# Optimization experiments

Measured on AMD Instinct MI355X. Metric: run time of the kernel, lower is better.

The kernel has to match this reference:

```python
import jax, jax.numpy as jnp
import numpy as np


def setup_inputs() -> dict:
    key = jax.random.key(0)
    k1, k2, k3, k4, k5 = jax.random.split(key, 5)
    N, K, F, N_up = 300000, 6, 64, 75000
    features = jax.random.normal(k1, (N, F), dtype=jnp.float32)
    weight = jax.random.uniform(k2, (N, 1), dtype=jnp.float32)
    nweights = jax.random.uniform(k3, (N, K), dtype=jnp.float32)
    nidx = jax.random.randint(k4, (N, K), 0, N, dtype=jnp.int32)
    sel_idx_up = jax.random.randint(k5, (N_up, 1), 0, N, dtype=jnp.int32)
    return {"features": features, "weight": weight, "nweights": nweights,
            "nidx": nidx, "sel_idx_up": sel_idx_up}


def reference(features, weight, nweights, nidx, sel_idx_up):
    # PushUp(mode='mean', add_self=False) with weight provided.
    N, F = features.shape
    w = jax.nn.relu(weight)                      # weights forced >= 0
    up_f = features * w                          # [N, F]
    up_f = jnp.concatenate([w, up_f], axis=-1)   # mean mode: prepend weight channel -> [N, F+1]

    # push_sum: each node i pushes nweights[i,k] * up_f[i] to node nidx[i,k]
    valid = (nidx >= 0)                          # -1 entries are masked (none here, kept for fidelity)
    safe_idx = jnp.where(valid, nidx, 0)         # [N, K]
    contrib = (nweights * valid.astype(up_f.dtype))[..., None] * up_f[:, None, :]  # [N, K, F+1]
    pushed = jnp.zeros((N, F + 1), dtype=up_f.dtype).at[safe_idx.reshape(-1)].add(
        contrib.reshape(-1, F + 1))              # [N, F+1]

    # gather_nd with depth-1 indices == gather along axis 0
    sel = pushed[sel_idx_up[:, 0]]               # [N_up, F+1]

    # tf.math.divide_no_nan(sel[:,1:], sel[:,0:1] + 0.001)
    denom = sel[:, 0:1] + 0.001
    safe_denom = jnp.where(denom == 0, 1.0, denom)
    out = jnp.where(denom == 0, 0.0, sel[:, 1:] / safe_denom)  # [N_up, F]
    return out
```

## Files before the change

### kernel.cpp

```cpp
#include <hip/hip_runtime.h>


#define KNB 6
#define FDIM 64
#define CAP 32
#define GB 4
#define EB 4

__global__ void mark_kernel(const int* __restrict__ sel,
                            int* __restrict__ cnt,
                            int Nup) {
    const int u = blockIdx.x * blockDim.x + threadIdx.x;
    if (u < Nup) cnt[sel[u]] = 0;
}

__global__ void build_kernel(const float* __restrict__ weight,
                             const float* __restrict__ nweights,
                             const int*   __restrict__ nidx,
                             int* __restrict__ cnt,
                             int2* __restrict__ table,
                             int E) {
    const int t  = blockIdx.x * blockDim.x + threadIdx.x;
    const int e0 = t * EB;
    if (e0 >= E) return;

    const int4   i4 = *(const int4*)(nidx + e0);
    const float4 n4 = *(const float4*)(nweights + e0);
    const int   idx[EB] = {i4.x, i4.y, i4.z, i4.w};
    const float nw [EB] = {n4.x, n4.y, n4.z, n4.w};

    int c[EB];
    #pragma unroll
    for (int j = 0; j < EB; ++j)
        c[j] = (idx[j] >= 0) ? cnt[idx[j]] : -1;

    #pragma unroll
    for (int j = 0; j < EB; ++j) {
        if (c[j] >= 0) {
            const int slot = atomicAdd(&cnt[idx[j]], 1);
            if (slot < CAP) {
                const int e = e0 + j;
                const int i = e / KNB;
                float w = weight[i];
                w = w > 0.0f ? w : 0.0f;
                table[(size_t)idx[j] * CAP + slot] =
                    make_int2(i, __float_as_int(nw[j] * w));
            }
        }
    }
}

__global__ void gather_kernel(const float* __restrict__ features,
                              const int*   __restrict__ sel,
                              const int*   __restrict__ cnt,
                              const int2*  __restrict__ table,
                              float* __restrict__ out,
                              int Nup) {
    const int wave = blockIdx.x * (blockDim.x >> 6) + (threadIdx.x >> 6);
    const int f    = threadIdx.x & 63;
    const int u0   = wave * GB;
    if (u0 >= Nup) return;

    int s[GB];
    #pragma unroll
    for (int j = 0; j < GB; ++j)
        s[j] = sel[(u0 + j < Nup) ? (u0 + j) : u0];
    int c[GB];
    #pragma unroll
    for (int j = 0; j < GB; ++j) c[j] = cnt[s[j]];

    int4 tr[GB][4];
    #pragma unroll
    for (int j = 0; j < GB; ++j) {
        const int4* row = (const int4*)(table + (size_t)s[j] * CAP);
        #pragma unroll
        for (int q = 0; q < 4; ++q) tr[j][q] = row[q];
    }

    float acc[GB], dsum[GB];
    #pragma unroll
    for (int j = 0; j < GB; ++j) {
        c[j] = c[j] < 0 ? 0 : (c[j] > CAP ? CAP : c[j]);
        acc[j] = 0.0f; dsum[j] = 0.0f;
    }

    #pragma unroll
    for (int j = 0; j < GB; ++j) {
        #pragma unroll
        for (int q = 0; q < 4; ++q) {
            const bool v0 = (2 * q    ) < c[j];
            const bool v1 = (2 * q + 1) < c[j];
            const int   src0 = v0 ? tr[j][q].x : 0;
            const int   src1 = v1 ? tr[j][q].z : 0;
            const float wn0  = v0 ? __int_as_float(tr[j][q].y) : 0.0f;
            const float wn1  = v1 ? __int_as_float(tr[j][q].w) : 0.0f;
            const float f0 = features[(size_t)src0 * FDIM + f];
            const float f1 = features[(size_t)src1 * FDIM + f];
            acc[j]  = fmaf(wn0, f0, acc[j]);
            acc[j]  = fmaf(wn1, f1, acc[j]);
            dsum[j] += wn0 + wn1;
        }
        for (int q = 8; q < c[j]; ++q) {
            const int2 tt = table[(size_t)s[j] * CAP + q];
            const float wn = __int_as_float(tt.y);
            acc[j]  = fmaf(wn, features[(size_t)tt.x * FDIM + f], acc[j]);
            dsum[j] += wn;
        }
    }

    #pragma unroll
    for (int j = 0; j < GB; ++j) {
        if (u0 + j < Nup) {
            const float d = dsum[j] + 0.001f;
            out[(size_t)(u0 + j) * FDIM + f] = acc[j] / d;
        }
    }
}

extern "C" void kernel_launch(void* const* d_in, const int* in_sizes, int n_in,
                              void* d_out, int out_size, void* d_ws, size_t ws_size,
                              hipStream_t stream) {
    const float* features = (const float*)d_in[0];
    const float* weight   = (const float*)d_in[1];
    const float* nweights = (const float*)d_in[2];
    const int*   nidx     = (const int*)d_in[3];
    const int*   sel      = (const int*)d_in[4];

    const int N   = in_sizes[1];
    const int Nup = in_sizes[4];
    const int E   = N * KNB;

    int*  cnt   = (int*)d_ws;
    int2* table = (int2*)(cnt + N);

    hipMemsetAsync(cnt, 0xC0, (size_t)N * sizeof(int), stream);

    const int T = 256;
    mark_kernel<<<(Nup + T - 1) / T, T, 0, stream>>>(sel, cnt, Nup);

    const int nthreads_build = (E + EB - 1) / EB;
    build_kernel<<<(nthreads_build + T - 1) / T, T, 0, stream>>>(
        weight, nweights, nidx, cnt, table, E);

    const int waves  = (Nup + GB - 1) / GB;
    const int wpb    = T / 64;
    const int blocks = (waves + wpb - 1) / wpb;
    gather_kernel<<<blocks, T, 0, stream>>>(features, sel, cnt, table,
                                            (float*)d_out, Nup);
}
```

Before: 205.3 us.

## Vectorize gather with float4 lanes over 8 nodes per wave; drop count memset

The gather kernel now splits each wave into four 16-lane groups. Each group handles two output nodes and loads features as float4, so a wave covers 8 nodes and issues all 16 feature-row loads up front. The goal is more memory-level parallelism and wider loads. The memset that set every count to a negative sentinel is removed, which leaves counts for unselected nodes with stale or uninitialized workspace values. The build kernel may then issue atomics and table writes for those nodes as well, which adds contention and traffic in exchange for skipping the memset.

```diff
diff --git a/kernel.cpp b/kernel.cpp
--- a/kernel.cpp
+++ b/kernel.cpp
@@ -4,7 +4,6 @@
 #define KNB 6
 #define FDIM 64
 #define CAP 32
-#define GB 4
 #define EB 4
 
 __global__ void mark_kernel(const int* __restrict__ sel,
@@ -57,63 +56,90 @@
                               float* __restrict__ out,
                               int Nup) {
     const int wave = blockIdx.x * (blockDim.x >> 6) + (threadIdx.x >> 6);
-    const int f    = threadIdx.x & 63;
-    const int u0   = wave * GB;
+    const int lane = threadIdx.x & 63;
+    const int q    = lane >> 4;
+    const int l    = lane & 15;
+    const int u0   = wave * 8;
     if (u0 >= Nup) return;
 
-    int s[GB];
+    const float4* feat4 = (const float4*)features;
+
+    const int uA = u0 + q;
+    const int uB = u0 + 4 + q;
+    const int uAc = (uA < Nup) ? uA : (Nup - 1);
+    const int uBc = (uB < Nup) ? uB : (Nup - 1);
+
+    const int sA = sel[uAc];
+    const int sB = sel[uBc];
+    int cA = cnt[sA], cB = cnt[sB];
+    const int4* rowA = (const int4*)(table + (size_t)sA * CAP);
+    const int4* rowB = (const int4*)(table + (size_t)sB * CAP);
+    int4 tA[4], tB[4];
     #pragma unroll
-    for (int j = 0; j < GB; ++j)
-        s[j] = sel[(u0 + j < Nup) ? (u0 + j) : u0];
-    int c[GB];
+    for (int p = 0; p < 4; ++p) { tA[p] = rowA[p]; tB[p] = rowB[p]; }
+
+    cA = cA < 0 ? 0 : (cA > CAP ? CAP : cA);
+    cB = cB < 0 ? 0 : (cB > CAP ? CAP : cB);
+
+    int   srcA[8], srcB[8];
+    float wnA[8],  wnB[8];
     #pragma unroll
-    for (int j = 0; j < GB; ++j) c[j] = cnt[s[j]];
-
-    int4 tr[GB][4];
+    for (int p = 0; p < 4; ++p) {
+        srcA[2*p]   = tA[p].x; wnA[2*p]   = __int_as_float(tA[p].y);
+        srcA[2*p+1] = tA[p].z; wnA[2*p+1] = __int_as_float(tA[p].w);
+        srcB[2*p]   = tB[p].x; wnB[2*p]   = __int_as_float(tB[p].y);
+        srcB[2*p+1] = tB[p].z; wnB[2*p+1] = __int_as_float(tB[p].w);
+    }
     #pragma unroll
-    for (int j = 0; j < GB; ++j) {
-        const int4* row = (const int4*)(table + (size_t)s[j] * CAP);
-        #pragma unroll
-        for (int q = 0; q < 4; ++q) tr[j][q] = row[q];
+    for (int j = 0; j < 8; ++j) {
+        const bool vA = j < cA, vB = j < cB;
+        srcA[j] = vA ? srcA[j] : 0;  wnA[j] = vA ? wnA[j] : 0.0f;
+        srcB[j] = vB ? srcB[j] : 0;  wnB[j] = vB ? wnB[j] : 0.0f;
     }
 
-    float acc[GB], dsum[GB];
+    float4 fA[8], fB[8];
     #pragma unroll
-    for (int j = 0; j < GB; ++j) {
-        c[j] = c[j] < 0 ? 0 : (c[j] > CAP ? CAP : c[j]);
-        acc[j] = 0.0f; dsum[j] = 0.0f;
+    for (int j = 0; j < 8; ++j) fA[j] = feat4[(size_t)srcA[j] * 16 + l];
+    #pragma unroll
+    for (int j = 0; j < 8; ++j) fB[j] = feat4[(size_t)srcB[j] * 16 + l];
+
+    float4 aA = make_float4(0.f,0.f,0.f,0.f), aB = make_float4(0.f,0.f,0.f,0.f);
+    float dA = 0.f, dB = 0.f;
+    #pragma unroll
+    for (int j = 0; j < 8; ++j) {
+        aA.x = fmaf(wnA[j], fA[j].x, aA.x); aA.y = fmaf(wnA[j], fA[j].y, aA.y);
+        aA.z = fmaf(wnA[j], fA[j].z, aA.z); aA.w = fmaf(wnA[j], fA[j].w, aA.w);
+        dA += wnA[j];
+        aB.x = fmaf(wnB[j], fB[j].x, aB.x); aB.y = fmaf(wnB[j], fB[j].y, aB.y);
+        aB.z = fmaf(wnB[j], fB[j].z, aB.z); aB.w = fmaf(wnB[j], fB[j].w, aB.w);
+        dB += wnB[j];
+    }
+    for (int j = 8; j < cA; ++j) {
+        const int2 tt = table[(size_t)sA * CAP + j];
+        const float wn = __int_as_float(tt.y);
+        const float4 fx = feat4[(size_t)tt.x * 16 + l];
+        aA.x = fmaf(wn, fx.x, aA.x); aA.y = fmaf(wn, fx.y, aA.y);
+        aA.z = fmaf(wn, fx.z, aA.z); aA.w = fmaf(wn, fx.w, aA.w);
+        dA += wn;
+    }
+    for (int j = 8; j < cB; ++j) {
+        const int2 tt = table[(size_t)sB * CAP + j];
+        const float wn = __int_as_float(tt.y);
+        const float4 fx = feat4[(size_t)tt.x * 16 + l];
+        aB.x = fmaf(wn, fx.x, aB.x); aB.y = fmaf(wn, fx.y, aB.y);
+        aB.z = fmaf(wn, fx.z, aB.z); aB.w = fmaf(wn, fx.w, aB.w);
+        dB += wn;
     }
 
-    #pragma unroll
-    for (int j = 0; j < GB; ++j) {
-        #pragma unroll
-        for (int q = 0; q < 4; ++q) {
-            const bool v0 = (2 * q    ) < c[j];
-            const bool v1 = (2 * q + 1) < c[j];
-            const int   src0 = v0 ? tr[j][q].x : 0;
-            const int   src1 = v1 ? tr[j][q].z : 0;
-            const float wn0  = v0 ? __int_as_float(tr[j][q].y) : 0.0f;
-            const float wn1  = v1 ? __int_as_float(tr[j][q].w) : 0.0f;
-            const float f0 = features[(size_t)src0 * FDIM + f];
-            const float f1 = features[(size_t)src1 * FDIM + f];
-            acc[j]  = fmaf(wn0, f0, acc[j]);
-            acc[j]  = fmaf(wn1, f1, acc[j]);
-            dsum[j] += wn0 + wn1;
-        }
-        for (int q = 8; q < c[j]; ++q) {
-            const int2 tt = table[(size_t)s[j] * CAP + q];
-            const float wn = __int_as_float(tt.y);
-            acc[j]  = fmaf(wn, features[(size_t)tt.x * FDIM + f], acc[j]);
-            dsum[j] += wn;
-        }
+    if (uA < Nup) {
+        const float d = dA + 0.001f;
+        ((float4*)out)[(size_t)uA * 16 + l] =
+            make_float4(aA.x/d, aA.y/d, aA.z/d, aA.w/d);
     }
-
-    #pragma unroll
-    for (int j = 0; j < GB; ++j) {
-        if (u0 + j < Nup) {
-            const float d = dsum[j] + 0.001f;
-            out[(size_t)(u0 + j) * FDIM + f] = acc[j] / d;
-        }
+    if (uB < Nup) {
+        const float d = dB + 0.001f;
+        ((float4*)out)[(size_t)uB * 16 + l] =
+            make_float4(aB.x/d, aB.y/d, aB.z/d, aB.w/d);
     }
 }
 
@@ -133,16 +159,14 @@
     int*  cnt   = (int*)d_ws;
     int2* table = (int2*)(cnt + N);
 
-    hipMemsetAsync(cnt, 0xC0, (size_t)N * sizeof(int), stream);
-
     const int T = 256;
     mark_kernel<<<(Nup + T - 1) / T, T, 0, stream>>>(sel, cnt, Nup);
 
-    const int nthreads_build = (E + EB - 1) / EB;
+    const int nthreads_build = E / EB;
     build_kernel<<<(nthreads_build + T - 1) / T, T, 0, stream>>>(
         weight, nweights, nidx, cnt, table, E);
 
-    const int waves  = (Nup + GB - 1) / GB;
+    const int waves  = (Nup + 7) / 8;
     const int wpb    = T / 64;
     const int blocks = (waves + wpb - 1) / wpb;
     gather_kernel<<<blocks, T, 0, stream>>>(features, sel, cnt, table,
```

Result: faster. 184.2 us (-10.3%).
